# Kernel tuning notes

Measured on AMD Instinct MI355X. Metric: run time of the kernel, lower is better.

## Reference

```python
import jax, jax.numpy as jnp
import numpy as np

N_EMBD = 1024
N_HEAD = 16
HEAD_DIM = N_EMBD // N_HEAD  # 64; scale = sqrt(64) = 8


def setup_inputs() -> dict:
    key = jax.random.key(0)
    k0, k1, k2, k3, k4 = jax.random.split(key, 5)
    B, T = 4, 2048
    x = jax.random.normal(k0, (B, T, N_EMBD), dtype=jnp.float32)
    # torch Linear weights are (out,in); we store (in,out) so y = x @ W + b
    W_attn = jax.random.normal(k1, (N_EMBD, 3 * N_EMBD), dtype=jnp.float32) * 0.02
    b_attn = jax.random.normal(k2, (3 * N_EMBD,), dtype=jnp.float32) * 0.02
    W_proj = jax.random.normal(k3, (N_EMBD, N_EMBD), dtype=jnp.float32) * 0.02
    b_proj = jax.random.normal(k4, (N_EMBD,), dtype=jnp.float32) * 0.02
    return {"x": x, "W_attn": W_attn, "b_attn": b_attn,
            "W_proj": W_proj, "b_proj": b_proj}


def reference(x, W_attn, b_attn, W_proj, b_proj):
    B, T, D = x.shape
    scale = 1.0 / np.float32(np.sqrt(HEAD_DIM))
    qkv = x @ W_attn + b_attn                      # [B,T,3D]
    q, k, v = jnp.split(qkv, 3, axis=-1)           # each [B,T,D]
    att = jnp.einsum('bid,bjd->bij', q, k) * scale # [B,T,T]
    causal = jnp.tril(jnp.ones((T, T), dtype=bool))
    att = jnp.where(causal[None, :, :], att, jnp.float32(-jnp.inf))
    att = jax.nn.softmax(att, axis=-1)
    y = jnp.einsum('bij,bjd->bid', att, v)         # [B,T,D]
    return y @ W_proj + b_proj
```

## Files before the change

kernel.cpp:

```cpp
#include <hip/hip_runtime.h>

typedef __attribute__((ext_vector_type(8))) short short8;
typedef __attribute__((ext_vector_type(4))) float f32x4;
typedef __attribute__((ext_vector_type(4))) unsigned short ushort4v;

struct DB0 { static constexpr int value = 0; };
struct DB1 { static constexpr int value = 1; };

__device__ __forceinline__ unsigned short f2bf(float f) {
  unsigned int u = __float_as_uint(f);
  u += 0x7fffu + ((u >> 16) & 1u);
  return (unsigned short)(u >> 16);
}
__device__ __forceinline__ float bf2f(unsigned short h) {
  return __uint_as_float(((unsigned int)h) << 16);
}

__device__ __forceinline__ void gload16(const unsigned short* g, unsigned short* l) {
  __builtin_amdgcn_global_load_lds(
      (const __attribute__((address_space(1))) unsigned int*)g,
      (__attribute__((address_space(3))) unsigned int*)l,
      16, 0, 0);
}

template <int OFF>
__device__ __forceinline__ short8 dsr(unsigned a) {
  short8 r;
  asm volatile("ds_read_b128 %0, %1 offset:%2" : "=v"(r) : "v"(a), "n"(OFF));
  return r;
}

__device__ __forceinline__ void bar() {
  asm volatile("" ::: "memory");
  __builtin_amdgcn_s_barrier();
  asm volatile("" ::: "memory");
}

__global__ __launch_bounds__(256) void prep_kernel(
    const float* __restrict__ x, unsigned short* __restrict__ xb,
    const float* __restrict__ Wa, unsigned short* __restrict__ wta,
    const float* __restrict__ Wp, unsigned short* __restrict__ wtp) {
  int b = blockIdx.x;
  int tx = threadIdx.x & 31, ty = threadIdx.x >> 5;
  if (b < 8192) {
    int i = b * 256 + threadIdx.x;
    f32x4 v = ((const f32x4*)x)[i];
    ushort4v o;
    o[0] = f2bf(v[0]); o[1] = f2bf(v[1]); o[2] = f2bf(v[2]); o[3] = f2bf(v[3]);
    ((ushort4v*)xb)[i] = o;
    return;
  }
  const float* W; unsigned short* Wt; int K, N, n0, k0;
  if (b < 8192 + 3072) {
    int bb = b - 8192; W = Wa; Wt = wta; K = 1024; N = 3072;
    n0 = (bb % 96) * 32; k0 = (bb / 96) * 32;
  } else {
    int bb = b - 11264; W = Wp; Wt = wtp; K = 1024; N = 1024;
    n0 = (bb % 32) * 32; k0 = (bb / 32) * 32;
  }
  __shared__ float tile[32][33];
#pragma unroll
  for (int j = 0; j < 32; j += 8)
    tile[ty + j][tx] = W[(size_t)(k0 + ty + j) * N + n0 + tx];
  __syncthreads();
#pragma unroll
  for (int j = 0; j < 32; j += 8)
    Wt[(size_t)(n0 + ty + j) * K + k0 + tx] = f2bf(tile[tx][ty + j]);
}

__global__ __launch_bounds__(256) void softmax_kernel(unsigned short* __restrict__ S) {
  int row = blockIdx.x * 4 + (threadIdx.x >> 6);
  int l = threadIdx.x & 63;
  int rl = row & 2047;
  int rend = ((rl >> 7) + 1) << 7;
  unsigned short* p = S + (size_t)row * 2048;
  float v[32];
  float mx = -3e38f;
#pragma unroll
  for (int i = 0; i < 4; i++) {
    int c0 = (i * 64 + l) * 8;
    if (c0 < rend) {
      short8 raw = *(const short8*)&p[c0];
#pragma unroll
      for (int j = 0; j < 8; j++) {
        v[i * 8 + j] = bf2f((unsigned short)raw[j]);
        mx = fmaxf(mx, v[i * 8 + j]);
      }
    } else {
#pragma unroll
      for (int j = 0; j < 8; j++) v[i * 8 + j] = -3e38f;
    }
  }
#pragma unroll
  for (int off = 1; off < 64; off <<= 1) mx = fmaxf(mx, __shfl_xor(mx, off));
  float s = 0.f;
#pragma unroll
  for (int i = 0; i < 32; i++) { v[i] = exp2f((v[i] - mx) * 1.44269504f); s += v[i]; }
#pragma unroll
  for (int off = 1; off < 64; off <<= 1) s += __shfl_xor(s, off);
  float inv = 1.f / s;
#pragma unroll
  for (int i = 0; i < 4; i++) {
    int c0 = (i * 64 + l) * 8;
    if (c0 < rend) {
      short8 o;
#pragma unroll
      for (int j = 0; j < 8; j++) o[j] = (short)f2bf(v[i * 8 + j] * inv);
      *(short8*)&p[c0] = o;
    }
  }
}

template <int OUTBF>
__device__ __forceinline__ void gemm_body(
    unsigned short (*lds)[16384],
    const unsigned short* __restrict__ A, int lda,
    const unsigned short* __restrict__ Bt, int ldb,
    void* __restrict__ Cv, int ldc,
    const float* __restrict__ bias, int NT, float scale, bool maskC,
    int m0, int n0) {
  const int t = threadIdx.x;
  const int lane = t & 63, wid = t >> 6;
  const int g = lane >> 4, q = lane & 15;
  const int wm = wid >> 1, wn = wid & 1;

  f32x4 acc[4][4] = {};

  {
    const int scol = ((t & 7) * 8) ^ ((t & 32) >> 1);
    const unsigned short* aS = A + (size_t)(m0 + (t >> 3)) * lda + scol;
    const unsigned short* bS = Bt + (size_t)(n0 + (t >> 3)) * ldb + scol;

    auto stage = [&](int tt) {
      unsigned short* d = &lds[tt & 1][wid * 512];
      const unsigned short* sa = aS + (size_t)tt * 64;
      const unsigned short* sb = bS + (size_t)tt * 64;
      gload16(sa, d);
      gload16(sa + (size_t)32 * lda, d + 2048);
      gload16(sa + (size_t)64 * lda, d + 4096);
      gload16(sa + (size_t)96 * lda, d + 6144);
      gload16(sb, d + 8192);
      gload16(sb + (size_t)32 * ldb, d + 10240);
      gload16(sb + (size_t)64 * ldb, d + 12288);
      gload16(sb + (size_t)96 * ldb, d + 14336);
    };

    const unsigned base =
        (unsigned)(unsigned long long)(__attribute__((address_space(3))) unsigned short*)&lds[0][0];
    const int colA = (g * 16) ^ ((q & 4) << 3);
    const unsigned aaB = base + (unsigned)((wm * 64 + q) * 128 + colA);
    const unsigned bbB = base + 16384u + (unsigned)((wn * 64 + q) * 128 + colA);

    stage(0);
    asm volatile("s_waitcnt vmcnt(0)" ::: "memory");
    bar();

    auto body = [&](auto dbc, int tt) {
      constexpr int DB = decltype(dbc)::value;
      const unsigned aa = aaB + DB * 32768u;
      const unsigned bb = bbB + DB * 32768u;
      if (tt + 1 < NT) stage(tt + 1);
      short8 aq[4][2], bq[4][2];
#pragma unroll
      for (int m = 0; m < 4; m++) {
        aq[m][0] = dsr<0>(aa + m * 2048u);
        aq[m][1] = dsr<64>(aa + m * 2048u);
      }
#pragma unroll
      for (int n = 0; n < 4; n++) {
        bq[n][0] = dsr<0>(bb + n * 2048u);
        bq[n][1] = dsr<64>(bb + n * 2048u);
      }
      asm volatile("s_waitcnt lgkmcnt(0)" ::: "memory");
      __builtin_amdgcn_sched_barrier(0);
      __builtin_amdgcn_s_setprio(1);
#pragma unroll
      for (int ks = 0; ks < 2; ks++)
#pragma unroll
        for (int m = 0; m < 4; m++)
#pragma unroll
          for (int n = 0; n < 4; n++)
            acc[m][n] = __builtin_amdgcn_mfma_f32_16x16x32_bf16(aq[m][ks], bq[n][ks], acc[m][n], 0, 0, 0);
      __builtin_amdgcn_s_setprio(0);
      __builtin_amdgcn_sched_barrier(0);
      asm volatile("s_waitcnt vmcnt(0)" ::: "memory");
      bar();
    };

    int tt = 0;
    for (; tt + 2 <= NT; tt += 2) {
      body(DB0{}, tt);
      body(DB1{}, tt + 1);
    }
    if (tt < NT) body(DB0{}, tt);
  }

#pragma unroll
  for (int n = 0; n < 4; n++) {
    int colg = n0 + wn * 64 + n * 16 + q;
    float bv = bias ? bias[colg] : 0.f;
#pragma unroll
    for (int m = 0; m < 4; m++) {
      int rowb = m0 + wm * 64 + m * 16 + g * 4;
#pragma unroll
      for (int r = 0; r < 4; r++) {
        float val = acc[m][n][r] * scale + bv;
        if (maskC && colg > rowb + r) val = -1e30f;
        if (OUTBF) {
          ((unsigned short*)Cv)[(size_t)(rowb + r) * ldc + colg] = f2bf(val);
        } else {
          ((float*)Cv)[(size_t)(rowb + r) * ldc + colg] = val;
        }
      }
    }
  }
}

template <int OUTBF>
__global__ __launch_bounds__(256) void gemm128_kernel(
    const unsigned short* __restrict__ A, int lda, long long saz,
    const unsigned short* __restrict__ Bt, int ldb, long long sbz,
    void* __restrict__ Cv, int ldc, long long scz,
    const float* __restrict__ bias, int K, float scale, int causal) {
  __shared__ __align__(16) unsigned short lds[2][16384];
  int bx, by, z;
  if (causal == 4) {
    int gx = gridDim.x, gy = gridDim.y, gz = gridDim.z;
    int total = gx * gy * gz;
    int id = blockIdx.x + blockIdx.y * gx + blockIdx.z * gx * gy;
    int halfn = total >> 1;
    int half = id >= halfn;
    int r = id - half * halfn;
    bx = r % gx;
    int rest = r / gx;
    int by0 = rest % gy;
    z = rest / gy + half * (gz >> 1);
    by = half ? (gy - 1 - by0) : by0;
  } else {
    bx = blockIdx.x; by = blockIdx.y; z = blockIdx.z;
  }
  const int m0 = by * 128, n0 = bx * 128;
  int NT = K >> 6;
  if (causal == 4) NT = min(K, m0 + 128) >> 6;
  char* C = (char*)Cv + (size_t)z * scz * (OUTBF ? 2 : 4);
  gemm_body<OUTBF>(lds, A + (size_t)z * saz, lda, Bt + (size_t)z * sbz, ldb,
                   C, ldc, bias, NT, scale, false, m0, n0);
}

__global__ __launch_bounds__(256) void gemm_sv_kernel(
    const unsigned short* __restrict__ qkv,
    const unsigned short* __restrict__ wtp,
    unsigned short* __restrict__ S,
    unsigned short* __restrict__ vt) {
  __shared__ __align__(16) unsigned short lds[2][16384];
  int i = blockIdx.x;
  if (i < 512) {
    int bx = i & 15, by = (i >> 4) & 7, z = i >> 7;
    gemm_body<1>(lds, wtp, 1024,
                 qkv + 2048 + (size_t)z * 2048 * 3072, 3072,
                 vt + (size_t)z * 1024 * 2048, 2048,
                 nullptr, 16, 1.0f, false, by * 128, bx * 128);
  } else {
    int ii = i - 512;
    int z = ii / 136, tri = ii % 136;
    int by = (int)((sqrtf(8.f * tri + 1.f) - 1.f) * 0.5f);
    while ((by + 1) * (by + 2) / 2 <= tri) by++;
    while (by * (by + 1) / 2 > tri) by--;
    int bx = tri - by * (by + 1) / 2;
    gemm_body<1>(lds, qkv + (size_t)z * 2048 * 3072, 3072,
                 qkv + 1024 + (size_t)z * 2048 * 3072, 3072,
                 S + (size_t)z * 2048 * 2048, 2048,
                 nullptr, 16, 0.125f, true, by * 128, bx * 128);
  }
}

extern "C" void kernel_launch(void* const* d_in, const int* in_sizes, int n_in,
                              void* d_out, int out_size, void* d_ws, size_t ws_size,
                              hipStream_t stream) {
  const float* x  = (const float*)d_in[0];
  const float* Wa = (const float*)d_in[1];
  const float* ba = (const float*)d_in[2];
  const float* Wp = (const float*)d_in[3];
  const float* bp = (const float*)d_in[4];
  float* out = (float*)d_out;

  char* ws = (char*)d_ws;
  unsigned short* qkv = (unsigned short*)(ws);
  unsigned short* xb  = (unsigned short*)(ws + 50331648);
  unsigned short* vt  = (unsigned short*)(ws + 50331648);
  unsigned short* wta = (unsigned short*)(ws + 67108864);
  unsigned short* S   = (unsigned short*)(ws + 73400320);
  unsigned short* wtp = (unsigned short*)(ws + 123731968);

  prep_kernel<<<12288, 256, 0, stream>>>(x, xb, Wa, wta, Wp, wtp);

  gemm128_kernel<1><<<dim3(24, 64, 1), 256, 0, stream>>>(
      xb, 1024, 0, wta, 1024, 0, qkv, 3072, 0, ba, 1024, 1.0f, 0);

  gemm_sv_kernel<<<1056, 256, 0, stream>>>(qkv, wtp, S, vt);

  softmax_kernel<<<2048, 256, 0, stream>>>(S);

  gemm128_kernel<0><<<dim3(8, 16, 4), 256, 0, stream>>>(
      S, 2048, 2048LL * 2048, vt, 2048, 2048LL * 1024,
      out, 1024, 2048LL * 1024, bp, 2048, 1.0f, 4);
}
```

Before: 185.1 us.

## Use K=32 triple-buffered GEMM body in fused S/V kernel for occupancy

Adds a GEMM body with a 32-wide K tile and three LDS buffers (48KB total instead of 64KB), used for both the V-transpose projection and the causal QK^T score GEMM. The launch bound now asks for 3 blocks per CU, aiming to raise occupancy and hide load latency with deeper prefetch. The cost is twice as many K iterations, each with a barrier and fewer MFMAs between syncs.

```diff
diff --git a/kernel.cpp b/kernel.cpp
--- a/kernel.cpp
+++ b/kernel.cpp
@@ -6,6 +6,7 @@
 
 struct DB0 { static constexpr int value = 0; };
 struct DB1 { static constexpr int value = 1; };
+struct DB2 { static constexpr int value = 2; };
 
 __device__ __forceinline__ unsigned short f2bf(float f) {
   unsigned int u = __float_as_uint(f);
@@ -211,6 +212,100 @@
         } else {
           ((float*)Cv)[(size_t)(rowb + r) * ldc + colg] = val;
         }
+      }
+    }
+  }
+}
+
+__device__ __forceinline__ void gemm_body32(
+    unsigned short (*lds)[8192],
+    const unsigned short* __restrict__ A, int lda,
+    const unsigned short* __restrict__ Bt, int ldb,
+    unsigned short* __restrict__ C, int ldc,
+    int NT, float scale, bool maskC, int m0, int n0) {
+  const int t = threadIdx.x;
+  const int lane = t & 63, wid = t >> 6;
+  const int g = lane >> 4, q = lane & 15;
+  const int wm = wid >> 1, wn = wid & 1;
+
+  f32x4 acc[4][4] = {};
+
+  {
+    const int scol = ((t & 3) ^ ((t >> 3) & 3)) * 8;
+    const unsigned short* aS = A + (size_t)(m0 + (t >> 2)) * lda + scol;
+    const unsigned short* bS = Bt + (size_t)(n0 + (t >> 2)) * ldb + scol;
+
+    auto stage = [&](int tt, int buf) {
+      unsigned short* d = &lds[buf][wid * 512];
+      const unsigned short* sa = aS + (size_t)tt * 32;
+      const unsigned short* sb = bS + (size_t)tt * 32;
+      gload16(sa, d);
+      gload16(sa + (size_t)64 * lda, d + 2048);
+      gload16(sb, d + 4096);
+      gload16(sb + (size_t)64 * ldb, d + 6144);
+    };
+
+    const unsigned base =
+        (unsigned)(unsigned long long)(__attribute__((address_space(3))) unsigned short*)&lds[0][0];
+    const int cb = ((g ^ ((q >> 1) & 3)) << 4);
+    const unsigned aaB = base + (unsigned)((wm * 64 + q) * 64 + cb);
+    const unsigned bbB = base + 8192u + (unsigned)((wn * 64 + q) * 64 + cb);
+
+    stage(0, 0);
+
+    auto body = [&](auto dbc, int tt) {
+      constexpr int DB = decltype(dbc)::value;
+      if (tt + 1 < NT) {
+        stage(tt + 1, (DB + 1) % 3);
+        asm volatile("s_waitcnt vmcnt(4)" ::: "memory");
+      } else {
+        asm volatile("s_waitcnt vmcnt(0)" ::: "memory");
+      }
+      bar();
+      const unsigned aa = aaB + DB * 16384u;
+      const unsigned bb = bbB + DB * 16384u;
+      short8 aq[4], bq[4];
+      aq[0] = dsr<0>(aa);
+      aq[1] = dsr<1024>(aa);
+      aq[2] = dsr<2048>(aa);
+      aq[3] = dsr<3072>(aa);
+      bq[0] = dsr<0>(bb);
+      bq[1] = dsr<1024>(bb);
+      bq[2] = dsr<2048>(bb);
+      bq[3] = dsr<3072>(bb);
+      asm volatile("s_waitcnt lgkmcnt(0)" ::: "memory");
+      __builtin_amdgcn_sched_barrier(0);
+      __builtin_amdgcn_s_setprio(1);
+#pragma unroll
+      for (int m = 0; m < 4; m++)
+#pragma unroll
+        for (int n = 0; n < 4; n++)
+          acc[m][n] = __builtin_amdgcn_mfma_f32_16x16x32_bf16(aq[m], bq[n], acc[m][n], 0, 0, 0);
+      __builtin_amdgcn_s_setprio(0);
+      __builtin_amdgcn_sched_barrier(0);
+    };
+
+    int tt = 0;
+    for (; tt + 3 <= NT; tt += 3) {
+      body(DB0{}, tt);
+      body(DB1{}, tt + 1);
+      body(DB2{}, tt + 2);
+    }
+    if (tt < NT) body(DB0{}, tt);
+    if (tt + 1 < NT) body(DB1{}, tt + 1);
+  }
+
+#pragma unroll
+  for (int n = 0; n < 4; n++) {
+    int colg = n0 + wn * 64 + n * 16 + q;
+#pragma unroll
+    for (int m = 0; m < 4; m++) {
+      int rowb = m0 + wm * 64 + m * 16 + g * 4;
+#pragma unroll
+      for (int r = 0; r < 4; r++) {
+        float val = acc[m][n][r] * scale;
+        if (maskC && colg > rowb + r) val = -1e30f;
+        C[(size_t)(rowb + r) * ldc + colg] = f2bf(val);
       }
     }
   }
@@ -247,19 +342,19 @@
                    C, ldc, bias, NT, scale, false, m0, n0);
 }
 
-__global__ __launch_bounds__(256) void gemm_sv_kernel(
+__global__ __launch_bounds__(256, 3) void gemm_sv_kernel(
     const unsigned short* __restrict__ qkv,
     const unsigned short* __restrict__ wtp,
     unsigned short* __restrict__ S,
     unsigned short* __restrict__ vt) {
-  __shared__ __align__(16) unsigned short lds[2][16384];
+  __shared__ __align__(16) unsigned short lds[3][8192];
   int i = blockIdx.x;
   if (i < 512) {
     int bx = i & 15, by = (i >> 4) & 7, z = i >> 7;
-    gemm_body<1>(lds, wtp, 1024,
-                 qkv + 2048 + (size_t)z * 2048 * 3072, 3072,
-                 vt + (size_t)z * 1024 * 2048, 2048,
-                 nullptr, 16, 1.0f, false, by * 128, bx * 128);
+    gemm_body32(lds, wtp, 1024,
+                qkv + 2048 + (size_t)z * 2048 * 3072, 3072,
+                vt + (size_t)z * 1024 * 2048, 2048,
+                32, 1.0f, false, by * 128, bx * 128);
   } else {
     int ii = i - 512;
     int z = ii / 136, tri = ii % 136;
@@ -267,10 +362,10 @@
     while ((by + 1) * (by + 2) / 2 <= tri) by++;
     while (by * (by + 1) / 2 > tri) by--;
     int bx = tri - by * (by + 1) / 2;
-    gemm_body<1>(lds, qkv + (size_t)z * 2048 * 3072, 3072,
-                 qkv + 1024 + (size_t)z * 2048 * 3072, 3072,
-                 S + (size_t)z * 2048 * 2048, 2048,
-                 nullptr, 16, 0.125f, true, by * 128, bx * 128);
+    gemm_body32(lds, qkv + (size_t)z * 2048 * 3072, 3072,
+                qkv + 1024 + (size_t)z * 2048 * 3072, 3072,
+                S + (size_t)z * 2048 * 2048, 2048,
+                32, 0.125f, true, by * 128, bx * 128);
   }
 }
 
```

Measured after the change: 184.5 us (median of 2 runs). About the same (-0.3%).
